# Kernel optimization log

Hardware: AMD Instinct MI355X
Metric: run time of the kernel (lower is better)

Reference implementation:

```python
import jax, jax.numpy as jnp
import numpy as np

B, S = 8, 512                  # batch, seq_len
V, H, L = 30522, 768, 12       # vocab, hidden, layers
NH, F, T, P = 12, 3072, 2, 512 # heads, ffn dim, type vocab, max positions
D = H // NH
EPS = 1e-12


def layer_norm(x, scale, bias):
    mu = jnp.mean(x, axis=-1, keepdims=True)
    var = jnp.mean((x - mu) ** 2, axis=-1, keepdims=True)
    return (x - mu) * jax.lax.rsqrt(var + EPS) * scale + bias


def setup_inputs() -> dict:
    key = jax.random.key(0)
    ks = jax.random.split(key, 16)
    p = lambda k, shp: (0.02 * jax.random.normal(k, shp, dtype=jnp.float32))
    return {
        "input_ids": jax.random.randint(ks[0], (B, S), 0, V, dtype=jnp.int32),
        "type_ids": jax.random.randint(ks[1], (B, S), 0, T, dtype=jnp.int32),
        "word_emb": p(ks[2], (V, H)),
        "pos_emb": p(ks[3], (P, H)),
        "type_emb": p(ks[4], (T, H)),
        "emb_ln_scale": jnp.ones((H,), jnp.float32),
        "emb_ln_bias": jnp.zeros((H,), jnp.float32),
        "wq": p(ks[5], (L, H, H)), "bq": jnp.zeros((L, H), jnp.float32),
        "wk": p(ks[6], (L, H, H)), "bk": jnp.zeros((L, H), jnp.float32),
        "wv": p(ks[7], (L, H, H)), "bv": jnp.zeros((L, H), jnp.float32),
        "wo": p(ks[8], (L, H, H)), "bo": jnp.zeros((L, H), jnp.float32),
        "ln1_scale": jnp.ones((L, H), jnp.float32), "ln1_bias": jnp.zeros((L, H), jnp.float32),
        "w1": p(ks[9], (L, H, F)), "b1": jnp.zeros((L, F), jnp.float32),
        "w2": p(ks[10], (L, F, H)), "b2": jnp.zeros((L, H), jnp.float32),
        "ln2_scale": jnp.ones((L, H), jnp.float32), "ln2_bias": jnp.zeros((L, H), jnp.float32),
    }


def reference(input_ids, type_ids, word_emb, pos_emb, type_emb, emb_ln_scale,
              emb_ln_bias, wq, bq, wk, bk, wv, bv, wo, bo, ln1_scale, ln1_bias,
              w1, b1, w2, b2, ln2_scale, ln2_bias):
    # padding mask: 1.0 where token id == 0, shape [B,1,1,S]
    mask = (input_ids == 0).astype(jnp.float32)[:, None, None, :]
    # embeddings: word + position + segment, then layernorm (dropout off / eval)
    h = word_emb[input_ids] + pos_emb[None, :S, :] + type_emb[type_ids]
    h = layer_norm(h, emb_ln_scale, emb_ln_bias)

    def block(x, lp):
        (wq_, bq_, wk_, bk_, wv_, bv_, wo_, bo_, l1s, l1b,
         w1_, b1_, w2_, b2_, l2s, l2b) = lp
        def heads(y, w, b):  # [B,S,H] -> [B,NH,S,D]
            return (y @ w + b).reshape(B, S, NH, D).transpose(0, 2, 1, 3)
        q = heads(x, wq_, bq_)
        k = heads(x, wk_, bk_)
        v = heads(x, wv_, bv_)
        logits = jnp.einsum('bhqd,bhkd->bhqk', q, k) / jnp.sqrt(jnp.float32(D))
        logits = logits + mask * -10000.0
        attn = jax.nn.softmax(logits, axis=-1)
        ctx = jnp.einsum('bhqk,bhkd->bhqd', attn, v)
        ctx = ctx.transpose(0, 2, 1, 3).reshape(B, S, H)
        x = layer_norm(x + ctx @ wo_ + bo_, l1s, l1b)
        ffn = jax.nn.gelu(x @ w1_ + b1_, approximate=False) @ w2_ + b2_
        x = layer_norm(x + ffn, l2s, l2b)
        return x, None

    h, _ = jax.lax.scan(block, h, (wq, bq, wk, bk, wv, bv, wo, bo,
                                   ln1_scale, ln1_bias, w1, b1, w2, b2,
                                   ln2_scale, ln2_bias))
    return h
```

## Files before the change

### kernel.cpp

```cpp
#include <hip/hip_runtime.h>
#include <hip/hip_bf16.h>
#include <math.h>

#define S_LEN   512
#define HID     768
#define NLAYER  12
#define NHEAD   12
#define FFN_DIM 3072
#define HDIM    64
#define NTOK    4096
#define QKVN    2304

typedef __bf16 bf16x8 __attribute__((ext_vector_type(8)));
typedef float  f32x4  __attribute__((ext_vector_type(4)));
typedef unsigned short us8 __attribute__((ext_vector_type(8)));

#define MFMA16(a, b, c) __builtin_amdgcn_mfma_f32_16x16x32_bf16((a), (b), (c), 0, 0, 0)

__device__ __forceinline__ void block_reduce_2(float& sum, float& sq) {
  __shared__ float sd[8];
  int lane = threadIdx.x & 63;
  int wid  = threadIdx.x >> 6;
  #pragma unroll
  for (int off = 32; off > 0; off >>= 1) {
    sum += __shfl_down(sum, off, 64);
    sq  += __shfl_down(sq,  off, 64);
  }
  if (lane == 0) { sd[wid] = sum; sd[4 + wid] = sq; }
  __syncthreads();
  sum = sd[0] + sd[1] + sd[2] + sd[3];
  sq  = sd[4] + sd[5] + sd[6] + sd[7];
}

__global__ __launch_bounds__(256) void mask_kernel(const int* __restrict__ ids,
                                                   float* __restrict__ mb) {
  int i = blockIdx.x * 256 + threadIdx.x;
  if (i < NTOK) mb[i] = (ids[i] == 0) ? -10000.0f : 0.0f;
}

__global__ __launch_bounds__(256) void embed_ln_kernel(
    const int* __restrict__ ids, const int* __restrict__ tids,
    const float* __restrict__ we, const float* __restrict__ pe,
    const float* __restrict__ te, const float* __restrict__ gamma,
    const float* __restrict__ beta, float* __restrict__ out32,
    __bf16* __restrict__ out16) {
  int t = blockIdx.x;
  int s = t & (S_LEN - 1);
  int id = ids[t];
  int tp = tids[t];
  float x[3];
  #pragma unroll
  for (int i = 0; i < 3; ++i) {
    int c = threadIdx.x + i * 256;
    x[i] = we[(size_t)id * HID + c] + pe[(size_t)s * HID + c] +
           te[(size_t)tp * HID + c];
  }
  float sum = x[0] + x[1] + x[2];
  float sq  = x[0]*x[0] + x[1]*x[1] + x[2]*x[2];
  block_reduce_2(sum, sq);
  float mu   = sum * (1.0f / HID);
  float var  = sq * (1.0f / HID) - mu * mu;
  float rstd = rsqrtf(var + 1e-12f);
  #pragma unroll
  for (int i = 0; i < 3; ++i) {
    int c = threadIdx.x + i * 256;
    float v = (x[i] - mu) * rstd * gamma[c] + beta[c];
    out32[(size_t)t * HID + c] = v;
    out16[(size_t)t * HID + c] = (__bf16)v;
  }
}

__global__ __launch_bounds__(256) void add_ln_kernel(
    const float* __restrict__ a, const float* __restrict__ b,
    const float* __restrict__ gamma, const float* __restrict__ beta,
    float* __restrict__ out32, __bf16* __restrict__ out16) {
  int t = blockIdx.x;
  float x[3];
  #pragma unroll
  for (int i = 0; i < 3; ++i) {
    int c = threadIdx.x + i * 256;
    size_t idx = (size_t)t * HID + c;
    x[i] = a[idx] + b[idx];
  }
  float sum = x[0] + x[1] + x[2];
  float sq  = x[0]*x[0] + x[1]*x[1] + x[2]*x[2];
  block_reduce_2(sum, sq);
  float mu   = sum * (1.0f / HID);
  float var  = sq * (1.0f / HID) - mu * mu;
  float rstd = rsqrtf(var + 1e-12f);
  #pragma unroll
  for (int i = 0; i < 3; ++i) {
    int c = threadIdx.x + i * 256;
    float v = (x[i] - mu) * rstd * gamma[c] + beta[c];
    out32[(size_t)t * HID + c] = v;
    out16[(size_t)t * HID + c] = (__bf16)v;
  }
}

__global__ __launch_bounds__(256) void tcvt_kernel(
    const float* __restrict__ src, __bf16* __restrict__ dst, int R, int C) {
  __shared__ float tile[32][33];
  int c0 = blockIdx.x * 32, r0 = blockIdx.y * 32;
  int tx = threadIdx.x & 31, ty = threadIdx.x >> 5;
  #pragma unroll
  for (int i = 0; i < 4; ++i) {
    int r = ty + i * 8;
    tile[r][tx] = src[(size_t)(r0 + r) * C + c0 + tx];
  }
  __syncthreads();
  #pragma unroll
  for (int i = 0; i < 4; ++i) {
    int r = ty + i * 8;
    dst[(size_t)(c0 + r) * R + r0 + tx] = (__bf16)tile[tx][r];
  }
}

__global__ __launch_bounds__(256) void vtrans_kernel(
    const __bf16* __restrict__ qkv, __bf16* __restrict__ vt) {
  __shared__ __bf16 tile[32][33];
  int bh = blockIdx.z;
  int b = bh / NHEAD, h = bh % NHEAD;
  int s0 = blockIdx.x * 32, d0 = blockIdx.y * 32;
  int tx = threadIdx.x & 31, ty = threadIdx.x >> 5;
  #pragma unroll
  for (int i = 0; i < 4; ++i) {
    int r = ty + i * 8;
    tile[r][tx] = qkv[(size_t)(b * S_LEN + s0 + r) * QKVN + 2 * HID + h * HDIM + d0 + tx];
  }
  __syncthreads();
  #pragma unroll
  for (int i = 0; i < 4; ++i) {
    int r = ty + i * 8;
    vt[((size_t)bh * HDIM + d0 + r) * S_LEN + s0 + tx] = tile[tx][r];
  }
}

template <int MODE>
__global__ __launch_bounds__(256) void mfma_gemm(
    const __bf16* __restrict__ A, const __bf16* __restrict__ Bt,
    const float* __restrict__ bias, void* __restrict__ Cout,
    int M, int N, int K) {
  constexpr int LDT = 72;
  __shared__ __align__(16) __bf16 As[128 * LDT];
  __shared__ __align__(16) __bf16 Bs[64 * LDT];
  const int tid  = threadIdx.x;
  const int wv   = tid >> 6;
  const int lane = tid & 63;
  const int l15  = lane & 15, quad = lane >> 4;
  const int m0 = blockIdx.y * 128, n0 = blockIdx.x * 64;
  const int srow = tid >> 3, schk = tid & 7;

  f32x4 acc[2][4];
  const f32x4 z4 = {0.f, 0.f, 0.f, 0.f};
  #pragma unroll
  for (int i = 0; i < 2; ++i)
    #pragma unroll
    for (int j = 0; j < 4; ++j) acc[i][j] = z4;

  const __bf16* Ag = A  + (size_t)(m0 + srow) * K + schk * 8;
  const __bf16* Bg = Bt + (size_t)(n0 + srow) * K + schk * 8;

  for (int kt = 0; kt < K; kt += 64) {
    #pragma unroll
    for (int c = 0; c < 4; ++c)
      *(us8*)&As[(srow + c * 32) * LDT + schk * 8] =
          *(const us8*)(Ag + (size_t)(c * 32) * K + kt);
    #pragma unroll
    for (int c = 0; c < 2; ++c)
      *(us8*)&Bs[(srow + c * 32) * LDT + schk * 8] =
          *(const us8*)(Bg + (size_t)(c * 32) * K + kt);
    __syncthreads();
    #pragma unroll
    for (int kc = 0; kc < 2; ++kc) {
      bf16x8 af[2], bfr[4];
      #pragma unroll
      for (int rt = 0; rt < 2; ++rt)
        af[rt] = *(const bf16x8*)&As[(wv * 32 + rt * 16 + l15) * LDT + kc * 32 + quad * 8];
      #pragma unroll
      for (int ct = 0; ct < 4; ++ct)
        bfr[ct] = *(const bf16x8*)&Bs[(ct * 16 + l15) * LDT + kc * 32 + quad * 8];
      #pragma unroll
      for (int rt = 0; rt < 2; ++rt)
        #pragma unroll
        for (int ct = 0; ct < 4; ++ct)
          acc[rt][ct] = MFMA16(af[rt], bfr[ct], acc[rt][ct]);
    }
    __syncthreads();
  }

  #pragma unroll
  for (int rt = 0; rt < 2; ++rt) {
    int rbase = m0 + wv * 32 + rt * 16 + quad * 4;
    #pragma unroll
    for (int ct = 0; ct < 4; ++ct) {
      int col = n0 + ct * 16 + l15;
      float bv = bias[col];
      #pragma unroll
      for (int r = 0; r < 4; ++r) {
        float v = acc[rt][ct][r] + bv;
        if (MODE == 2) v = 0.5f * v * (1.0f + erff(v * 0.70710678118654752f));
        if (MODE == 0)
          ((float*)Cout)[(size_t)(rbase + r) * N + col] = v;
        else
          ((__bf16*)Cout)[(size_t)(rbase + r) * N + col] = (__bf16)v;
      }
    }
  }
}

__global__ __launch_bounds__(256) void attn_mfma(
    const __bf16* __restrict__ qkv,
    const __bf16* __restrict__ vt,
    const float* __restrict__ mb,
    __bf16* __restrict__ ctx) {
  constexpr int PLD = 264;
  __shared__ __align__(16) __bf16 Plds[4][16 * PLD];
  const int tid = threadIdx.x;
  const int wv = tid >> 6, lane = tid & 63;
  const int l15 = lane & 15, quad = lane >> 4;
  const int b = blockIdx.z, hh = blockIdx.y, q0 = blockIdx.x * 64;
  const f32x4 z4 = {0.f, 0.f, 0.f, 0.f};

  size_t qoff = ((size_t)(b * S_LEN) + q0 + wv * 16 + l15) * QKVN + hh * HDIM;
  bf16x8 qa0 = *(const bf16x8*)(qkv + qoff + quad * 8);
  bf16x8 qa1 = *(const bf16x8*)(qkv + qoff + 32 + quad * 8);

  f32x4 sc[32];
  #pragma unroll
  for (int kt = 0; kt < 32; ++kt) {
    size_t koff = ((size_t)(b * S_LEN) + kt * 16 + l15) * QKVN + HID + hh * HDIM;
    bf16x8 kb0 = *(const bf16x8*)(qkv + koff + quad * 8);
    bf16x8 kb1 = *(const bf16x8*)(qkv + koff + 32 + quad * 8);
    f32x4 t = MFMA16(qa0, kb0, z4);
    sc[kt] = MFMA16(qa1, kb1, t);
  }

  float mx[4] = {-1e30f, -1e30f, -1e30f, -1e30f};
  #pragma unroll
  for (int kt = 0; kt < 32; ++kt) {
    float mval = mb[b * S_LEN + kt * 16 + l15];
    #pragma unroll
    for (int r = 0; r < 4; ++r) {
      float x = sc[kt][r] * 0.125f + mval;
      sc[kt][r] = x;
      mx[r] = fmaxf(mx[r], x);
    }
  }
  #pragma unroll
  for (int m = 1; m < 16; m <<= 1)
    #pragma unroll
    for (int r = 0; r < 4; ++r) mx[r] = fmaxf(mx[r], __shfl_xor(mx[r], m, 64));

  float sm[4] = {0.f, 0.f, 0.f, 0.f};
  #pragma unroll
  for (int kt = 0; kt < 32; ++kt)
    #pragma unroll
    for (int r = 0; r < 4; ++r) {
      float e = __expf(sc[kt][r] - mx[r]);
      sc[kt][r] = e;
      sm[r] += e;
    }
  #pragma unroll
  for (int m = 1; m < 16; m <<= 1)
    #pragma unroll
    for (int r = 0; r < 4; ++r) sm[r] += __shfl_xor(sm[r], m, 64);
  float inv[4];
  #pragma unroll
  for (int r = 0; r < 4; ++r) inv[r] = 1.0f / sm[r];

  __bf16* pbuf = &Plds[wv][0];
  const __bf16* vbase = vt + (size_t)(b * NHEAD + hh) * HDIM * S_LEN;
  f32x4 oc[4] = {z4, z4, z4, z4};
  #pragma unroll
  for (int half = 0; half < 2; ++half) {
    #pragma unroll
    for (int kt2 = 0; kt2 < 16; ++kt2) {
      int kt = half * 16 + kt2;
      #pragma unroll
      for (int r = 0; r < 4; ++r)
        pbuf[(quad * 4 + r) * PLD + kt2 * 16 + l15] = (__bf16)(sc[kt][r] * inv[r]);
    }
    #pragma unroll
    for (int kc = 0; kc < 8; ++kc) {
      bf16x8 pa = *(const bf16x8*)&pbuf[l15 * PLD + kc * 32 + quad * 8];
      int kbase = half * 256 + kc * 32;
      #pragma unroll
      for (int ct = 0; ct < 4; ++ct) {
        const __bf16* vp =
            vbase + (size_t)(ct * 16 + l15) * S_LEN + kbase + quad * 8;
        oc[ct] = MFMA16(pa, *(const bf16x8*)vp, oc[ct]);
      }
    }
  }

  int orow = b * S_LEN + q0 + wv * 16 + quad * 4;
  #pragma unroll
  for (int ct = 0; ct < 4; ++ct) {
    int col = hh * HDIM + ct * 16 + l15;
    #pragma unroll
    for (int r = 0; r < 4; ++r)
      ctx[(size_t)(orow + r) * HID + col] = (__bf16)oc[ct][r];
  }
}

extern "C" void kernel_launch(void* const* d_in, const int* in_sizes, int n_in,
                              void* d_out, int out_size, void* d_ws, size_t ws_size,
                              hipStream_t stream) {
  const int*   input_ids = (const int*)d_in[0];
  const int*   type_ids  = (const int*)d_in[1];
  const float* word_emb  = (const float*)d_in[2];
  const float* pos_emb   = (const float*)d_in[3];
  const float* type_emb  = (const float*)d_in[4];
  const float* eln_s     = (const float*)d_in[5];
  const float* eln_b     = (const float*)d_in[6];
  const float* wq = (const float*)d_in[7];
  const float* bq = (const float*)d_in[8];
  const float* wk = (const float*)d_in[9];
  const float* bk = (const float*)d_in[10];
  const float* wv = (const float*)d_in[11];
  const float* bv = (const float*)d_in[12];
  const float* wo = (const float*)d_in[13];
  const float* bo = (const float*)d_in[14];
  const float* l1s = (const float*)d_in[15];
  const float* l1b = (const float*)d_in[16];
  const float* w1  = (const float*)d_in[17];
  const float* b1  = (const float*)d_in[18];
  const float* w2  = (const float*)d_in[19];
  const float* b2  = (const float*)d_in[20];
  const float* l2s = (const float*)d_in[21];
  const float* l2b = (const float*)d_in[22];

  char* p = (char*)d_ws;
  float*   h32    = (float*)p;            p += (size_t)NTOK * HID * 4;
  float*   tmp32  = (float*)p;            p += (size_t)NTOK * HID * 4;
  __bf16*  vT16   = (__bf16*)tmp32;
  __bf16*  h16    = (__bf16*)p;           p += (size_t)NTOK * HID * 2;
  __bf16*  qkv16  = (__bf16*)p;           p += (size_t)NTOK * QKVN * 2;
  __bf16*  ctx16  = (__bf16*)p;           p += (size_t)NTOK * HID * 2;
  __bf16*  ffn16  = qkv16;
  __bf16*  wT     = (__bf16*)p;           p += (size_t)QKVN * HID * 2;
  __bf16*  woT    = (__bf16*)p;           p += (size_t)HID * HID * 2;
  __bf16*  w1T    = (__bf16*)p;           p += (size_t)HID * FFN_DIM * 2;
  __bf16*  w2T    = (__bf16*)p;           p += (size_t)HID * FFN_DIM * 2;
  float*   qkvb   = (float*)p;            p += (size_t)QKVN * 4;
  float*   mb     = (float*)p;            p += (size_t)NTOK * 4;

  dim3 blk(256);
  mask_kernel<<<dim3(NTOK / 256), blk, 0, stream>>>(input_ids, mb);
  embed_ln_kernel<<<dim3(NTOK), blk, 0, stream>>>(
      input_ids, type_ids, word_emb, pos_emb, type_emb, eln_s, eln_b, h32, h16);

  dim3 g_qkv(QKVN / 64, NTOK / 128);
  dim3 g_hh(HID / 64, NTOK / 128);
  dim3 g_hf(FFN_DIM / 64, NTOK / 128);
  dim3 g_at(S_LEN / 64, NHEAD, 8);
  dim3 g_t1(HID / 32, HID / 32);
  dim3 g_t2(FFN_DIM / 32, HID / 32);
  dim3 g_t3(HID / 32, FFN_DIM / 32);
  dim3 g_vt(S_LEN / 32, HDIM / 32, 8 * NHEAD);

  const size_t WHH = (size_t)HID * HID;
  const size_t WHF = (size_t)HID * FFN_DIM;

  for (int l = 0; l < NLAYER; ++l) {
    size_t boff = (size_t)l * HID;
    tcvt_kernel<<<g_t1, blk, 0, stream>>>(wq + l * WHH, wT,           HID, HID);
    tcvt_kernel<<<g_t1, blk, 0, stream>>>(wk + l * WHH, wT + WHH,     HID, HID);
    tcvt_kernel<<<g_t1, blk, 0, stream>>>(wv + l * WHH, wT + 2 * WHH, HID, HID);
    tcvt_kernel<<<g_t1, blk, 0, stream>>>(wo + l * WHH, woT,          HID, HID);
    tcvt_kernel<<<g_t2, blk, 0, stream>>>(w1 + l * WHF, w1T, HID, FFN_DIM);
    tcvt_kernel<<<g_t3, blk, 0, stream>>>(w2 + l * WHF, w2T, FFN_DIM, HID);
    hipMemcpyAsync(qkvb,            bq + boff, HID * 4, hipMemcpyDeviceToDevice, stream);
    hipMemcpyAsync(qkvb + HID,      bk + boff, HID * 4, hipMemcpyDeviceToDevice, stream);
    hipMemcpyAsync(qkvb + 2 * HID,  bv + boff, HID * 4, hipMemcpyDeviceToDevice, stream);

    mfma_gemm<1><<<g_qkv, blk, 0, stream>>>(h16, wT, qkvb, qkv16, NTOK, QKVN, HID);
    vtrans_kernel<<<g_vt, blk, 0, stream>>>(qkv16, vT16);
    attn_mfma<<<g_at, blk, 0, stream>>>(qkv16, vT16, mb, ctx16);
    mfma_gemm<0><<<g_hh, blk, 0, stream>>>(ctx16, woT, bo + boff, tmp32, NTOK, HID, HID);
    add_ln_kernel<<<dim3(NTOK), blk, 0, stream>>>(h32, tmp32, l1s + boff, l1b + boff, h32, h16);
    mfma_gemm<2><<<g_hf, blk, 0, stream>>>(h16, w1T, b1 + (size_t)l * FFN_DIM, ffn16,
                                           NTOK, FFN_DIM, HID);
    mfma_gemm<0><<<g_hh, blk, 0, stream>>>(ffn16, w2T, b2 + boff, tmp32, NTOK, HID, FFN_DIM);
    float* dst = (l == NLAYER - 1) ? (float*)d_out : h32;
    add_ln_kernel<<<dim3(NTOK), blk, 0, stream>>>(h32, tmp32, l2s + boff, l2b + boff, dst, h16);
  }
}
```

Measured before the change: 3.117 ms.

## Use direct global-to-LDS loads with XOR swizzle and 128x128 GEMM tiles

The MFMA GEMM now stages A and B tiles with global_load_lds (global memory straight into LDS, skipping VGPRs), using an XOR-swizzled, unpadded LDS layout to avoid bank conflicts. A template tile width lets the QKV and FFN1 GEMMs use 128x128 tiles with a 2x2 wave layout for more data reuse, while the narrow-N GEMMs keep 128x64. Also merges the four HxH weight transpose launches into one and packs all QKV biases once, replacing the three per-layer memcpys. Larger tiles raise register pressure and reduce the number of blocks. The loop is still single-buffered, so loads are not overlapped with compute.

```diff
diff --git a/kernel.cpp b/kernel.cpp
--- a/kernel.cpp
+++ b/kernel.cpp
@@ -15,6 +15,9 @@
 typedef float  f32x4  __attribute__((ext_vector_type(4)));
 typedef unsigned short us8 __attribute__((ext_vector_type(8)));
 
+typedef __attribute__((address_space(1))) const unsigned int gas_u32;
+typedef __attribute__((address_space(3))) unsigned int las_u32;
+
 #define MFMA16(a, b, c) __builtin_amdgcn_mfma_f32_16x16x32_bf16((a), (b), (c), 0, 0, 0)
 
 __device__ __forceinline__ void block_reduce_2(float& sum, float& sq) {
@@ -36,6 +39,18 @@
                                                    float* __restrict__ mb) {
   int i = blockIdx.x * 256 + threadIdx.x;
   if (i < NTOK) mb[i] = (ids[i] == 0) ? -10000.0f : 0.0f;
+}
+
+__global__ __launch_bounds__(256) void pack_qkvb_kernel(
+    const float* __restrict__ bq, const float* __restrict__ bk,
+    const float* __restrict__ bv, float* __restrict__ out) {
+  int i = blockIdx.x * 256 + threadIdx.x;
+  if (i >= NLAYER * QKVN) return;
+  int l = i / QKVN, c = i % QKVN;
+  float v = (c < HID) ? bq[l * HID + c]
+          : (c < 2 * HID) ? bk[l * HID + c - HID]
+                          : bv[l * HID + c - 2 * HID];
+  out[i] = v;
 }
 
 __global__ __launch_bounds__(256) void embed_ln_kernel(
@@ -115,6 +130,31 @@
   }
 }
 
+__global__ __launch_bounds__(256) void tcvt4_kernel(
+    const float* __restrict__ s0, const float* __restrict__ s1,
+    const float* __restrict__ s2, const float* __restrict__ s3,
+    __bf16* __restrict__ d0, __bf16* __restrict__ d1,
+    __bf16* __restrict__ d2, __bf16* __restrict__ d3) {
+  __shared__ float tile[32][33];
+  const float* src = (blockIdx.z == 0) ? s0 : (blockIdx.z == 1) ? s1
+                   : (blockIdx.z == 2) ? s2 : s3;
+  __bf16* dst = (blockIdx.z == 0) ? d0 : (blockIdx.z == 1) ? d1
+              : (blockIdx.z == 2) ? d2 : d3;
+  int c0 = blockIdx.x * 32, r0 = blockIdx.y * 32;
+  int tx = threadIdx.x & 31, ty = threadIdx.x >> 5;
+  #pragma unroll
+  for (int i = 0; i < 4; ++i) {
+    int r = ty + i * 8;
+    tile[r][tx] = src[(size_t)(r0 + r) * HID + c0 + tx];
+  }
+  __syncthreads();
+  #pragma unroll
+  for (int i = 0; i < 4; ++i) {
+    int r = ty + i * 8;
+    dst[(size_t)(c0 + r) * HID + r0 + tx] = (__bf16)tile[tx][r];
+  }
+}
+
 __global__ __launch_bounds__(256) void vtrans_kernel(
     const __bf16* __restrict__ qkv, __bf16* __restrict__ vt) {
   __shared__ __bf16 tile[32][33];
@@ -135,65 +175,79 @@
   }
 }
 
-template <int MODE>
+template <int MODE, int TN>
 __global__ __launch_bounds__(256) void mfma_gemm(
     const __bf16* __restrict__ A, const __bf16* __restrict__ Bt,
     const float* __restrict__ bias, void* __restrict__ Cout,
     int M, int N, int K) {
-  constexpr int LDT = 72;
-  __shared__ __align__(16) __bf16 As[128 * LDT];
-  __shared__ __align__(16) __bf16 Bs[64 * LDT];
-  const int tid  = threadIdx.x;
-  const int wv   = tid >> 6;
-  const int lane = tid & 63;
-  const int l15  = lane & 15, quad = lane >> 4;
-  const int m0 = blockIdx.y * 128, n0 = blockIdx.x * 64;
-  const int srow = tid >> 3, schk = tid & 7;
-
-  f32x4 acc[2][4];
+  constexpr int AI = 4;
+  constexpr int BI = TN / 32;
+  constexpr int RT = (TN == 128) ? 4 : 2;
+  constexpr int CT = 4;
+  __shared__ __align__(16) __bf16 As[128 * 64];
+  __shared__ __align__(16) __bf16 Bs[TN * 64];
+  const int tid = threadIdx.x;
+  const int w = tid >> 6, lane = tid & 63;
+  const int l15 = lane & 15, quad = lane >> 4;
+  const int m0 = blockIdx.y * 128, n0 = blockIdx.x * TN;
+  const int lr = lane >> 3;
+  const int colg = (lane & 7) ^ lr;
+
+  const int wr = (TN == 128) ? (w >> 1) * 64 : w * 32;
+  const int wc = (TN == 128) ? (w & 1) * 64 : 0;
+
+  f32x4 acc[RT][CT];
   const f32x4 z4 = {0.f, 0.f, 0.f, 0.f};
   #pragma unroll
-  for (int i = 0; i < 2; ++i)
-    #pragma unroll
-    for (int j = 0; j < 4; ++j) acc[i][j] = z4;
-
-  const __bf16* Ag = A  + (size_t)(m0 + srow) * K + schk * 8;
-  const __bf16* Bg = Bt + (size_t)(n0 + srow) * K + schk * 8;
+  for (int i = 0; i < RT; ++i)
+    #pragma unroll
+    for (int j = 0; j < CT; ++j) acc[i][j] = z4;
+
+  const __bf16* Ag = A  + (size_t)(m0 + 8 * AI * w + lr) * K + colg * 8;
+  const __bf16* Bg = Bt + (size_t)(n0 + 8 * BI * w + lr) * K + colg * 8;
+  __bf16* Al = As + 512 * AI * w;
+  __bf16* Bl = Bs + 512 * BI * w;
 
   for (int kt = 0; kt < K; kt += 64) {
     #pragma unroll
-    for (int c = 0; c < 4; ++c)
-      *(us8*)&As[(srow + c * 32) * LDT + schk * 8] =
-          *(const us8*)(Ag + (size_t)(c * 32) * K + kt);
-    #pragma unroll
-    for (int c = 0; c < 2; ++c)
-      *(us8*)&Bs[(srow + c * 32) * LDT + schk * 8] =
-          *(const us8*)(Bg + (size_t)(c * 32) * K + kt);
+    for (int i = 0; i < AI; ++i)
+      __builtin_amdgcn_global_load_lds(
+          (gas_u32*)(Ag + (size_t)(8 * i) * K + kt),
+          (las_u32*)(Al + 512 * i), 16, 0, 0);
+    #pragma unroll
+    for (int i = 0; i < BI; ++i)
+      __builtin_amdgcn_global_load_lds(
+          (gas_u32*)(Bg + (size_t)(8 * i) * K + kt),
+          (las_u32*)(Bl + 512 * i), 16, 0, 0);
     __syncthreads();
     #pragma unroll
     for (int kc = 0; kc < 2; ++kc) {
-      bf16x8 af[2], bfr[4];
-      #pragma unroll
-      for (int rt = 0; rt < 2; ++rt)
-        af[rt] = *(const bf16x8*)&As[(wv * 32 + rt * 16 + l15) * LDT + kc * 32 + quad * 8];
-      #pragma unroll
-      for (int ct = 0; ct < 4; ++ct)
-        bfr[ct] = *(const bf16x8*)&Bs[(ct * 16 + l15) * LDT + kc * 32 + quad * 8];
-      #pragma unroll
-      for (int rt = 0; rt < 2; ++rt)
+      bf16x8 af[RT], bfr[CT];
+      #pragma unroll
+      for (int rt = 0; rt < RT; ++rt) {
+        int row = wr + rt * 16 + l15;
+        af[rt] = *(const bf16x8*)&As[(row * 8 + ((kc * 4 + quad) ^ (row & 7))) * 8];
+      }
+      #pragma unroll
+      for (int ct = 0; ct < CT; ++ct) {
+        int col = wc + ct * 16 + l15;
+        bfr[ct] = *(const bf16x8*)&Bs[(col * 8 + ((kc * 4 + quad) ^ (col & 7))) * 8];
+      }
+      #pragma unroll
+      for (int rt = 0; rt < RT; ++rt)
         #pragma unroll
-        for (int ct = 0; ct < 4; ++ct)
+        for (int ct = 0; ct < CT; ++ct)
           acc[rt][ct] = MFMA16(af[rt], bfr[ct], acc[rt][ct]);
     }
     __syncthreads();
   }
 
   #pragma unroll
-  for (int rt = 0; rt < 2; ++rt) {
-    int rbase = m0 + wv * 32 + rt * 16 + quad * 4;
-    #pragma unroll
-    for (int ct = 0; ct < 4; ++ct) {
-      int col = n0 + ct * 16 + l15;
+  for (int rt = 0; rt < RT; ++rt) {
+    int rbase = m0 + wr + rt * 16 + quad * 4;
+    #pragma unroll
+    for (int ct = 0; ct < CT; ++ct) {
+      int col = n0 + wc + ct * 16 + l15;
       float bv = bias[col];
       #pragma unroll
       for (int r = 0; r < 4; ++r) {
@@ -342,19 +396,21 @@
   __bf16*  woT    = (__bf16*)p;           p += (size_t)HID * HID * 2;
   __bf16*  w1T    = (__bf16*)p;           p += (size_t)HID * FFN_DIM * 2;
   __bf16*  w2T    = (__bf16*)p;           p += (size_t)HID * FFN_DIM * 2;
-  float*   qkvb   = (float*)p;            p += (size_t)QKVN * 4;
+  float*   qkvb12 = (float*)p;            p += (size_t)NLAYER * QKVN * 4;
   float*   mb     = (float*)p;            p += (size_t)NTOK * 4;
 
   dim3 blk(256);
   mask_kernel<<<dim3(NTOK / 256), blk, 0, stream>>>(input_ids, mb);
+  pack_qkvb_kernel<<<dim3((NLAYER * QKVN + 255) / 256), blk, 0, stream>>>(
+      bq, bk, bv, qkvb12);
   embed_ln_kernel<<<dim3(NTOK), blk, 0, stream>>>(
       input_ids, type_ids, word_emb, pos_emb, type_emb, eln_s, eln_b, h32, h16);
 
-  dim3 g_qkv(QKVN / 64, NTOK / 128);
-  dim3 g_hh(HID / 64, NTOK / 128);
-  dim3 g_hf(FFN_DIM / 64, NTOK / 128);
+  dim3 g_qkv(QKVN / 128, NTOK / 128);
+  dim3 g_ff1(FFN_DIM / 128, NTOK / 128);
+  dim3 g_h64(HID / 64, NTOK / 128);
   dim3 g_at(S_LEN / 64, NHEAD, 8);
-  dim3 g_t1(HID / 32, HID / 32);
+  dim3 g_t4(HID / 32, HID / 32, 4);
   dim3 g_t2(FFN_DIM / 32, HID / 32);
   dim3 g_t3(HID / 32, FFN_DIM / 32);
   dim3 g_vt(S_LEN / 32, HDIM / 32, 8 * NHEAD);
@@ -364,25 +420,26 @@
 
   for (int l = 0; l < NLAYER; ++l) {
     size_t boff = (size_t)l * HID;
-    tcvt_kernel<<<g_t1, blk, 0, stream>>>(wq + l * WHH, wT,           HID, HID);
-    tcvt_kernel<<<g_t1, blk, 0, stream>>>(wk + l * WHH, wT + WHH,     HID, HID);
-    tcvt_kernel<<<g_t1, blk, 0, stream>>>(wv + l * WHH, wT + 2 * WHH, HID, HID);
-    tcvt_kernel<<<g_t1, blk, 0, stream>>>(wo + l * WHH, woT,          HID, HID);
+    tcvt4_kernel<<<g_t4, blk, 0, stream>>>(
+        wq + l * WHH, wk + l * WHH, wv + l * WHH, wo + l * WHH,
+        wT, wT + WHH, wT + 2 * WHH, woT);
     tcvt_kernel<<<g_t2, blk, 0, stream>>>(w1 + l * WHF, w1T, HID, FFN_DIM);
     tcvt_kernel<<<g_t3, blk, 0, stream>>>(w2 + l * WHF, w2T, FFN_DIM, HID);
-    hipMemcpyAsync(qkvb,            bq + boff, HID * 4, hipMemcpyDeviceToDevice, stream);
-    hipMemcpyAsync(qkvb + HID,      bk + boff, HID * 4, hipMemcpyDeviceToDevice, stream);
-    hipMemcpyAsync(qkvb + 2 * HID,  bv + boff, HID * 4, hipMemcpyDeviceToDevice, stream);
-
-    mfma_gemm<1><<<g_qkv, blk, 0, stream>>>(h16, wT, qkvb, qkv16, NTOK, QKVN, HID);
+
+    mfma_gemm<1, 128><<<g_qkv, blk, 0, stream>>>(
+        h16, wT, qkvb12 + (size_t)l * QKVN, qkv16, NTOK, QKVN, HID);
     vtrans_kernel<<<g_vt, blk, 0, stream>>>(qkv16, vT16);
     attn_mfma<<<g_at, blk, 0, stream>>>(qkv16, vT16, mb, ctx16);
-    mfma_gemm<0><<<g_hh, blk, 0, stream>>>(ctx16, woT, bo + boff, tmp32, NTOK, HID, HID);
-    add_ln_kernel<<<dim3(NTOK), blk, 0, stream>>>(h32, tmp32, l1s + boff, l1b + boff, h32, h16);
-    mfma_gemm<2><<<g_hf, blk, 0, stream>>>(h16, w1T, b1 + (size_t)l * FFN_DIM, ffn16,
-                                           NTOK, FFN_DIM, HID);
-    mfma_gemm<0><<<g_hh, blk, 0, stream>>>(ffn16, w2T, b2 + boff, tmp32, NTOK, HID, FFN_DIM);
+    mfma_gemm<0, 64><<<g_h64, blk, 0, stream>>>(
+        ctx16, woT, bo + boff, tmp32, NTOK, HID, HID);
+    add_ln_kernel<<<dim3(NTOK), blk, 0, stream>>>(
+        h32, tmp32, l1s + boff, l1b + boff, h32, h16);
+    mfma_gemm<2, 128><<<g_ff1, blk, 0, stream>>>(
+        h16, w1T, b1 + (size_t)l * FFN_DIM, ffn16, NTOK, FFN_DIM, HID);
+    mfma_gemm<0, 64><<<g_h64, blk, 0, stream>>>(
+        ffn16, w2T, b2 + boff, tmp32, NTOK, HID, FFN_DIM);
     float* dst = (l == NLAYER - 1) ? (float*)d_out : h32;
-    add_ln_kernel<<<dim3(NTOK), blk, 0, stream>>>(h32, tmp32, l2s + boff, l2b + boff, dst, h16);
-  }
-}
+    add_ln_kernel<<<dim3(NTOK), blk, 0, stream>>>(
+        h32, tmp32, l2s + boff, l2b + boff, dst, h16);
+  }
+}
```

Result: faster. 2.883 ms (-7.5%).
